# Kernel tuning notes

Hardware: AMD Instinct MI355X
Metric: run time of the kernel (lower is better)

Reference implementation:

```python
import jax, jax.numpy as jnp
import numpy as np

B, T, D, H = 8, 512, 1024, 16
DH = D // H
MAX_LEN = 512  # max_pos_encoding


def rel_pos_encoding(seq_len, dim):
    # Relative sinusoidal PE, full (non-causal) context, no hidden state.
    # positions: max_len-1 ... 1, 0, -1 ... -(max_len-1)
    pos = jnp.concatenate([
        jnp.arange(MAX_LEN - 1, 0, -1, dtype=jnp.float32),
        jnp.arange(0, -MAX_LEN, -1, dtype=jnp.float32),
    ])  # (2*max_len-1,)
    inv_freq = jnp.power(10000.0, -2.0 * jnp.arange(dim // 2, dtype=jnp.float32) / dim)
    ang = pos[:, None] * inv_freq[None, :]  # (2M-1, D/2)
    pe = jnp.zeros((2 * MAX_LEN - 1, dim), dtype=jnp.float32)
    pe = pe.at[:, 0::2].set(jnp.sin(ang)).at[:, 1::2].set(jnp.cos(ang))
    # non-causal slice: [max_len - seq_len : max_len - 1 + seq_len] -> 2T-1 rows
    return pe[MAX_LEN - seq_len: MAX_LEN - 1 + seq_len]


def rel_to_abs(s):
    # full-context skewing (Bello et al.): s is (B, H, T1, T2) with T2 = 2*T1 - 1
    b, h, t1, t2 = s.shape
    s = jnp.pad(s, ((0, 0), (0, 0), (0, 0), (0, 1)))
    s = s.reshape(b, h, t1 * (t2 + 1))
    s = jnp.pad(s, ((0, 0), (0, 0), (0, t2 - t1)))
    s = s.reshape(b, h, t1 + 1, t2)
    return s[:, :, :t1, t1 - 1:]  # (B, H, T1, T1)


def setup_inputs() -> dict:
    key = jax.random.key(0)
    ks = jax.random.split(key, 9)
    sc = 1.0 / np.sqrt(D)
    return {
        "x": jax.random.normal(ks[0], (B, T, D), dtype=jnp.float32),
        "Wq": jax.random.normal(ks[1], (D, D), dtype=jnp.float32) * sc,
        "bq": jnp.zeros((D,), dtype=jnp.float32),
        "Wk": jax.random.normal(ks[2], (D, D), dtype=jnp.float32) * sc,
        "bk": jnp.zeros((D,), dtype=jnp.float32),
        "Wv": jax.random.normal(ks[3], (D, D), dtype=jnp.float32) * sc,
        "bv": jnp.zeros((D,), dtype=jnp.float32),
        "Wp": jax.random.normal(ks[4], (D, D), dtype=jnp.float32) * sc,
        "bp": jnp.zeros((D,), dtype=jnp.float32),
        "Wo": jax.random.normal(ks[5], (D, D), dtype=jnp.float32) * sc,
        "bo": jnp.zeros((D,), dtype=jnp.float32),
        "u": jax.random.normal(ks[6], (D,), dtype=jnp.float32) * 0.02,
        "v": jax.random.normal(ks[7], (D,), dtype=jnp.float32) * 0.02,
    }


def reference(x, Wq, bq, Wk, bk, Wv, bv, Wp, bp, Wo, bo, u, v):
    b, t, d = x.shape
    Q = x @ Wq.T + bq
    K = x @ Wk.T + bk
    V = x @ Wv.T + bv
    Qu = Q + u
    Qv = Q + v
    # relative positional embeddings, projected: (2T-1, D)
    E = rel_pos_encoding(t, d) @ Wp.T + bp
    # split heads
    Qu = Qu.reshape(b, t, H, DH).transpose(0, 2, 1, 3)  # (B,H,T,dh)
    Qv = Qv.reshape(b, t, H, DH).transpose(0, 2, 1, 3)
    Kh = K.reshape(b, t, H, DH).transpose(0, 2, 1, 3)
    Vh = V.reshape(b, t, H, DH).transpose(0, 2, 1, 3)
    Eh = E.reshape(2 * t - 1, H, DH)  # (R,H,dh)
    att_scores_K = jnp.einsum("bhqd,bhkd->bhqk", Qu, Kh)
    att_scores_E = rel_to_abs(jnp.einsum("bhqd,rhd->bhqr", Qv, Eh))
    att_scores = (att_scores_K + att_scores_E) / jnp.sqrt(jnp.float32(DH))
    att_w = jax.nn.softmax(att_scores, axis=-1)
    O = jnp.einsum("bhqk,bhkd->bhqd", att_w, Vh)
    O = O.transpose(0, 2, 1, 3).reshape(b, t, d)
    return O @ Wo.T + bo
```

## Files before the change

### kernel.cpp

```cpp
#include <hip/hip_runtime.h>
#include <hip/hip_bf16.h>
#include <cmath>

using short8  = __attribute__((ext_vector_type(8))) short;
using f32x4   = __attribute__((ext_vector_type(4))) float;
using uint4v  = __attribute__((ext_vector_type(4))) unsigned;

#define DEV static __device__ __forceinline__

DEV unsigned short f2bf(float f) {
  union { float f; unsigned u; } v; v.f = f;
  unsigned r = v.u + 0x7FFFu + ((v.u >> 16) & 1u);
  return (unsigned short)(r >> 16);
}
DEV float bf2f(unsigned short b) {
  union { unsigned u; float f; } v; v.u = ((unsigned)b) << 16;
  return v.f;
}

DEV void async_copy16(const void* g, void* l) {
  __builtin_amdgcn_global_load_lds(
      (const __attribute__((address_space(1))) void*)g,
      (__attribute__((address_space(3))) void*)l, 16, 0, 0);
}

#define DPPF(x, ctrl)                                                     \
  __builtin_bit_cast(float, __builtin_amdgcn_update_dpp(                  \
      __builtin_bit_cast(int, (x)), __builtin_bit_cast(int, (x)), (ctrl), \
      0xF, 0xF, false))

DEV float rowmax16(float t) {
  t = fmaxf(t, DPPF(t, 0x128));
  t = fmaxf(t, DPPF(t, 0x124));
  t = fmaxf(t, DPPF(t, 0x122));
  t = fmaxf(t, DPPF(t, 0x121));
  return t;
}
DEV float rowsum16(float t) {
  t += DPPF(t, 0x128);
  t += DPPF(t, 0x124);
  t += DPPF(t, 0x122);
  t += DPPF(t, 0x121);
  return t;
}
DEV unsigned dpp_xor8(unsigned x) {
  return (unsigned)__builtin_amdgcn_update_dpp((int)x, (int)x, 0x128, 0xF, 0xF, false);
}

__global__ __launch_bounds__(256) void prep_kernel(
    const float* __restrict__ x,  const float* __restrict__ Wq,
    const float* __restrict__ Wk, const float* __restrict__ Wv,
    const float* __restrict__ Wp, const float* __restrict__ Wo,
    const float* __restrict__ bq, const float* __restrict__ bk,
    const float* __restrict__ bv,
    unsigned short* __restrict__ xb, unsigned short* __restrict__ Wqkvb,
    unsigned short* __restrict__ Wpb, unsigned short* __restrict__ Wob,
    unsigned short* __restrict__ peb, float* __restrict__ bqkv) {
  const int blk = blockIdx.x;
  const int tid = threadIdx.x;
  if (blk < 9216) {
    const float* src;
    unsigned short* dst;
    int i;
    if (blk < 4096) {
      src = x; dst = xb; i = blk * 256 + tid;
    } else {
      const int w = (blk - 4096) >> 10;
      i = ((blk - 4096) & 1023) * 256 + tid;
      if      (w == 0) { src = Wq; dst = Wqkvb; }
      else if (w == 1) { src = Wk; dst = Wqkvb + 1048576; }
      else if (w == 2) { src = Wv; dst = Wqkvb + 2097152; }
      else if (w == 3) { src = Wp; dst = Wpb; }
      else             { src = Wo; dst = Wob; }
    }
    float4 v = ((const float4*)src)[i];
    ushort4 o;
    o.x = f2bf(v.x); o.y = f2bf(v.y); o.z = f2bf(v.z); o.w = f2bf(v.w);
    ((ushort4*)dst)[i] = o;
  } else if (blk < 11264) {
    const int idx = (blk - 9216) * 256 + tid;
    const int r = idx >> 9;
    const int m = idx & 511;
    const float inv_freq = __expf((float)m * -0.017988946039016004f);
    const float ang = (float)(511 - r) * inv_freq;
    peb[(size_t)r * 1024 + 2 * m]     = f2bf(sinf(ang));
    peb[(size_t)r * 1024 + 2 * m + 1] = f2bf(cosf(ang));
  } else {
    const int i = (blk - 11264) * 256 + tid;
    const float* s = (i < 1024) ? bq : (i < 2048) ? bk : bv;
    bqkv[i] = s[i & 1023];
  }
}

template <int OUTF32>
DEV void gemm_tile(const unsigned short* __restrict__ A,
                   const unsigned short* __restrict__ B,
                   const float* __restrict__ bias, void* __restrict__ Cout,
                   int N, int K, int m0, int n0, int tid,
                   unsigned short* sA, unsigned short* sB) {
  const int lane = tid & 63;
  const int wave = tid >> 6;

  const unsigned short* gA[4];
  const unsigned short* gB[4];
  unsigned ldst[4];
#pragma unroll
  for (int it = 0; it < 4; ++it) {
    unsigned o = (unsigned)(it * 4096 + wave * 1024 + lane * 16);
    unsigned row = o >> 7;
    unsigned x = (o & 127u) ^ ((row & 7u) << 4);
    ldst[it] = it * 4096 + wave * 1024;
    gA[it] = A + (size_t)(m0 + (int)row) * K + (x >> 1);
    gB[it] = B + (size_t)(n0 + (int)row) * K + (x >> 1);
  }

  f32x4 acc[4][4];
#pragma unroll
  for (int i = 0; i < 4; ++i)
#pragma unroll
    for (int j = 0; j < 4; ++j) acc[i][j] = f32x4{0.f, 0.f, 0.f, 0.f};

  const int wm = (wave >> 1) << 6;
  const int wn = (wave & 1) << 6;
  const int rsel = lane & 15;
  const int g = lane >> 4;
  const int ksel = g << 4;

#pragma unroll
  for (int it = 0; it < 4; ++it) {
    async_copy16(gA[it], (char*)sA + ldst[it]);
    async_copy16(gB[it], (char*)sB + ldst[it]);
  }

  int cur = 0;
  for (int k0 = 0; k0 < K; k0 += 64) {
    __syncthreads();
    if (k0 + 64 < K) {
#pragma unroll
      for (int it = 0; it < 4; ++it) {
        async_copy16(gA[it] + k0 + 64, (char*)sA + (cur ^ 1) * 16384 + ldst[it]);
        async_copy16(gB[it] + k0 + 64, (char*)sB + (cur ^ 1) * 16384 + ldst[it]);
      }
    }
    const char* sAc = (const char*)sA + cur * 16384;
    const char* sBc = (const char*)sB + cur * 16384;
    __builtin_amdgcn_s_setprio(1);
#pragma unroll
    for (int kb = 0; kb < 2; ++kb) {
      const int kbyte = kb * 64 + ksel;
      short8 af[4], bf8[4];
#pragma unroll
      for (int i = 0; i < 4; ++i) {
        const int ra = wm + i * 16 + rsel;
        af[i] = *(const short8*)(sAc + ra * 128 + (kbyte ^ ((ra & 7) << 4)));
        const int rb = wn + i * 16 + rsel;
        bf8[i] = *(const short8*)(sBc + rb * 128 + (kbyte ^ ((rb & 7) << 4)));
      }
#pragma unroll
      for (int i = 0; i < 4; ++i)
#pragma unroll
        for (int j = 0; j < 4; ++j)
          acc[i][j] = __builtin_amdgcn_mfma_f32_16x16x32_bf16(bf8[j], af[i], acc[i][j], 0, 0, 0);
    }
    __builtin_amdgcn_s_setprio(0);
    cur ^= 1;
  }

#pragma unroll
  for (int i = 0; i < 4; ++i) {
    const int row = m0 + wm + i * 16 + rsel;
#pragma unroll
    for (int j = 0; j < 4; ++j) {
      const int col0 = n0 + wn + j * 16 + 4 * g;
      const float4 bb = *(const float4*)(bias + col0);
      if (OUTF32) {
        float4 o;
        o.x = acc[i][j][0] + bb.x;
        o.y = acc[i][j][1] + bb.y;
        o.z = acc[i][j][2] + bb.z;
        o.w = acc[i][j][3] + bb.w;
        *(float4*)&((float*)Cout)[(size_t)row * N + col0] = o;
      } else {
        ushort4 o;
        o.x = f2bf(acc[i][j][0] + bb.x);
        o.y = f2bf(acc[i][j][1] + bb.y);
        o.z = f2bf(acc[i][j][2] + bb.z);
        o.w = f2bf(acc[i][j][3] + bb.w);
        *(ushort4*)&((unsigned short*)Cout)[(size_t)row * N + col0] = o;
      }
    }
  }
}

__global__ __launch_bounds__(256) void gemm_qkv_e_kernel(
    const unsigned short* __restrict__ xb, const unsigned short* __restrict__ Wqkvb,
    const float* __restrict__ bqkv, unsigned short* __restrict__ QKVb,
    const unsigned short* __restrict__ peb, const unsigned short* __restrict__ Wpb,
    const float* __restrict__ bp, unsigned short* __restrict__ Eb) {
  __shared__ unsigned short sA[2 * 128 * 64];
  __shared__ unsigned short sB[2 * 128 * 64];
  const int cpx = 104;
  const int bid = (blockIdx.x & 7) * cpx + (blockIdx.x >> 3);
  if (bid < 768) {
    const int mt = bid / 24, nt = bid - mt * 24;
    gemm_tile<0>(xb, Wqkvb, bqkv, QKVb, 3072, 1024, mt << 7, nt << 7,
                 threadIdx.x, sA, sB);
  } else {
    const int b2 = bid - 768;
    gemm_tile<0>(peb, Wpb, bp, Eb, 1024, 1024, (b2 >> 3) << 7, (b2 & 7) << 7,
                 threadIdx.x, sA, sB);
  }
}

__global__ __launch_bounds__(256) void gemm_out_kernel(
    const unsigned short* __restrict__ Ob, const unsigned short* __restrict__ Wob,
    const float* __restrict__ bo, float* __restrict__ out) {
  __shared__ unsigned short sA[2 * 128 * 64];
  __shared__ unsigned short sB[2 * 128 * 64];
  const int cpx = 32;
  const int bid = (blockIdx.x & 7) * cpx + (blockIdx.x >> 3);
  gemm_tile<1>(Ob, Wob, bo, out, 1024, 1024, (bid >> 3) << 7, (bid & 7) << 7,
               threadIdx.x, sA, sB);
}

__global__ __launch_bounds__(256, 2) void attn_kernel(
    const unsigned short* __restrict__ QKV,
    const unsigned short* __restrict__ E,
    const float* __restrict__ uvec, const float* __restrict__ vvec,
    unsigned short* __restrict__ O) {
  __shared__ unsigned short sK[2 * 4096];
  __shared__ unsigned short sE[4 * 4096];
  __shared__ unsigned short sVt[2 * 4096];
  __shared__ unsigned short sP[4][2048];

  const int tid = threadIdx.x;
  const int lane = tid & 63;
  const int wave = tid >> 6;
  const int cpx = gridDim.x >> 3;
  const int bid = (blockIdx.x & 7) * cpx + (blockIdx.x >> 3);
  const int qt = bid & 3;
  const int h = (bid >> 2) & 15;
  const int b = bid >> 6;
  const int q0 = qt << 7;

  const int rsel = lane & 15;
  const int g = lane >> 4;
  const int ilocb = g << 2;
  const int cb0 = 96 - 32 * wave;

  const unsigned short* Qb = QKV + (size_t)b * 512 * 3072 + h * 64;
  const unsigned short* Kb = Qb + 1024;
  const unsigned short* Vb = Qb + 2048;

  const float sc = 0.125f * 1.44269504088896f;

  short8 v8b[2];
#pragma unroll
  for (int it = 0; it < 2; ++it) {
    const int c = it * 256 + tid;
    v8b[it] = *(const short8*)(Vb + (size_t)(c >> 3) * 3072 + ((c & 7) << 3));
  }
#pragma unroll
  for (int it = 0; it < 2; ++it) {
    const unsigned o = (unsigned)(it * 4096 + wave * 1024 + lane * 16);
    const unsigned row = o >> 7;
    const unsigned x = (o & 127u) ^ ((row & 7u) << 4);
    async_copy16(Kb + (size_t)row * 3072 + (x >> 1),
                 (char*)sK + it * 4096 + wave * 1024);
  }
#pragma unroll
  for (int hh = 0; hh < 3; ++hh) {
    const int H = 6 - 2 * qt + hh;
#pragma unroll
    for (int it = 0; it < 2; ++it) {
      const unsigned o = (unsigned)(it * 4096 + wave * 1024 + lane * 16);
      const unsigned row = o >> 7;
      const unsigned x = (o & 127u) ^ ((row & 7u) << 4);
      async_copy16(E + (size_t)(H * 64 + (int)row) * 1024 + h * 64 + (x >> 1),
                   (char*)sE + (H & 3) * 8192 + it * 4096 + wave * 1024);
    }
  }

  short8 aU[2][2], aV[2][2];
#pragma unroll
  for (int f = 0; f < 2; ++f) {
    const int qrow = q0 + 32 * wave + 16 * f + rsel;
    const int dob = g * 8;
#pragma unroll
    for (int kb = 0; kb < 2; ++kb) {
      short8 q8 = *(const short8*)(Qb + (size_t)qrow * 3072 + kb * 32 + dob);
#pragma unroll
      for (int j = 0; j < 8; ++j) {
        const float qf = bf2f((unsigned short)q8[j]);
        aU[f][kb][j] = (short)f2bf((qf + uvec[h * 64 + kb * 32 + dob + j]) * sc);
        aV[f][kb][j] = (short)f2bf((qf + vvec[h * 64 + kb * 32 + dob + j]) * sc);
      }
    }
  }

#pragma unroll
  for (int it = 0; it < 2; ++it) {
    const int c = it * 256 + tid;
    const int trow = c >> 3;
    const int db = (c & 7) << 3;
    const int odd = trow & 1;
    const int kp = (trow & ~1) * 2;
    const uint4v dw = __builtin_bit_cast(uint4v, v8b[it]);
#pragma unroll
    for (int p = 0; p < 4; ++p) {
      const unsigned mine = dw[p];
      const unsigned other = dpp_xor8(mine);
      const unsigned res = odd ? ((mine & 0xffff0000u) | (other >> 16))
                               : ((other << 16) | (mine & 0xffffu));
      const int d = db + 2 * p + odd;
      *(unsigned*)((char*)sVt + d * 128 + (kp ^ (((d ^ (d >> 3)) & 7) << 4))) = res;
    }
  }
#pragma unroll
  for (int it = 0; it < 2; ++it) {
    const int c = it * 256 + tid;
    v8b[it] = *(const short8*)(Vb + (size_t)(64 + (c >> 3)) * 3072 + ((c & 7) << 3));
  }

  int srcLn[4];
  bool hiSel[4];
#pragma unroll
  for (int r = 0; r < 4; ++r) {
    const int offs = 15 - (ilocb + r) + rsel;
    srcLn[r] = (lane & 48) | (offs & 15);
    hiSel[r] = offs >= 16;
  }

  float mrun[2][4], lrun[2][4];
  f32x4 oacc[2][4];
#pragma unroll
  for (int f = 0; f < 2; ++f)
#pragma unroll
    for (int r = 0; r < 4; ++r) { mrun[f][r] = -INFINITY; lrun[f][r] = 0.f; }
#pragma unroll
  for (int f = 0; f < 2; ++f)
#pragma unroll
    for (int n = 0; n < 4; ++n) oacc[f][n] = f32x4{0.f, 0.f, 0.f, 0.f};

  for (int kt = 0; kt < 8; ++kt) {
    const int k0 = kt << 6;
    const int cur = kt & 1;
    const int H0 = 6 - 2 * qt + kt;

    __syncthreads();

    if (kt < 7) {
      const int kn = k0 + 64;
#pragma unroll
      for (int it = 0; it < 2; ++it) {
        const unsigned o = (unsigned)(it * 4096 + wave * 1024 + lane * 16);
        const unsigned row = o >> 7;
        const unsigned x = (o & 127u) ^ ((row & 7u) << 4);
        async_copy16(Kb + (size_t)(kn + (int)row) * 3072 + (x >> 1),
                     (char*)sK + (cur ^ 1) * 8192 + it * 4096 + wave * 1024);
      }
      {
        const int H = H0 + 3;
#pragma unroll
        for (int it = 0; it < 2; ++it) {
          const unsigned o = (unsigned)(it * 4096 + wave * 1024 + lane * 16);
          const unsigned row = o >> 7;
          const unsigned x = (o & 127u) ^ ((row & 7u) << 4);
          async_copy16(E + (size_t)(H * 64 + (int)row) * 1024 + h * 64 + (x >> 1),
                       (char*)sE + (H & 3) * 8192 + it * 4096 + wave * 1024);
        }
      }
#pragma unroll
      for (int it = 0; it < 2; ++it) {
        const int c = it * 256 + tid;
        const int trow = c >> 3;
        const int db = (c & 7) << 3;
        const int odd = trow & 1;
        const int kp = (trow & ~1) * 2;
        const uint4v dw = __builtin_bit_cast(uint4v, v8b[it]);
#pragma unroll
        for (int p = 0; p < 4; ++p) {
          const unsigned mine = dw[p];
          const unsigned other = dpp_xor8(mine);
          const unsigned res = odd ? ((mine & 0xffff0000u) | (other >> 16))
                                   : ((other << 16) | (mine & 0xffffu));
          const int d = db + 2 * p + odd;
          *(unsigned*)((char*)sVt + (cur ^ 1) * 8192 + d * 128 +
                       (kp ^ (((d ^ (d >> 3)) & 7) << 4))) = res;
        }
      }
    }

    f32x4 skacc[2][4], gacc[2][5];
#pragma unroll
    for (int f = 0; f < 2; ++f) {
#pragma unroll
      for (int nf = 0; nf < 4; ++nf) skacc[f][nf] = f32x4{0.f, 0.f, 0.f, 0.f};
#pragma unroll
      for (int cf = 0; cf < 5; ++cf) gacc[f][cf] = f32x4{0.f, 0.f, 0.f, 0.f};
    }

    __builtin_amdgcn_s_setprio(1);
#pragma unroll
    for (int kb = 0; kb < 2; ++kb) {
      const int kbyte = kb * 64 + g * 16;
      const char* sKc = (const char*)sK + cur * 8192;
      short8 ka, kbb;
      {
        const int r0 = rsel, r1 = 16 + rsel;
        ka  = *(const short8*)(sKc + r0 * 128 + (kbyte ^ ((r0 & 7) << 4)));
        kbb = *(const short8*)(sKc + r1 * 128 + (kbyte ^ ((r1 & 7) << 4)));
      }
      skacc[0][0] = __builtin_amdgcn_mfma_f32_16x16x32_bf16(aU[0][kb], ka,  skacc[0][0], 0, 0, 0);
      skacc[1][0] = __builtin_amdgcn_mfma_f32_16x16x32_bf16(aU[1][kb], ka,  skacc[1][0], 0, 0, 0);
      skacc[0][1] = __builtin_amdgcn_mfma_f32_16x16x32_bf16(aU[0][kb], kbb, skacc[0][1], 0, 0, 0);
      skacc[1][1] = __builtin_amdgcn_mfma_f32_16x16x32_bf16(aU[1][kb], kbb, skacc[1][1], 0, 0, 0);
      {
        const int r0 = 32 + rsel, r1 = 48 + rsel;
        ka  = *(const short8*)(sKc + r0 * 128 + (kbyte ^ ((r0 & 7) << 4)));
        kbb = *(const short8*)(sKc + r1 * 128 + (kbyte ^ ((r1 & 7) << 4)));
      }
      skacc[0][2] = __builtin_amdgcn_mfma_f32_16x16x32_bf16(aU[0][kb], ka,  skacc[0][2], 0, 0, 0);
      skacc[1][2] = __builtin_amdgcn_mfma_f32_16x16x32_bf16(aU[1][kb], ka,  skacc[1][2], 0, 0, 0);
      skacc[0][3] = __builtin_amdgcn_mfma_f32_16x16x32_bf16(aU[0][kb], kbb, skacc[0][3], 0, 0, 0);
      skacc[1][3] = __builtin_amdgcn_mfma_f32_16x16x32_bf16(aU[1][kb], kbb, skacc[1][3], 0, 0, 0);
    }
    __builtin_amdgcn_sched_barrier(0);

    if (kt < 6) {
#pragma unroll
      for (int it = 0; it < 2; ++it) {
        const int c = it * 256 + tid;
        v8b[it] = *(const short8*)(Vb + (size_t)(k0 + 128 + (c >> 3)) * 3072 +
                                   ((c & 7) << 3));
      }
    }

#pragma unroll
    for (int kb = 0; kb < 2; ++kb) {
      const int kbyte = kb * 64 + g * 16;
      short8 e0, e1, e2;
#define LDE(cfu)                                                              \
  ({                                                                          \
    const int rowbase = cb0 + 16 * (cfu);                                     \
    const int rb = rowbase + rsel;                                            \
    const int slot = (H0 + (rowbase >> 6)) & 3;                               \
    *(const short8*)((const char*)sE + slot * 8192 + (rb & 63) * 128 +        \
                     (kbyte ^ ((rb & 7) << 4)));                              \
  })
      e0 = LDE(0); e1 = LDE(1); e2 = LDE(2);
      gacc[1][0] = __builtin_amdgcn_mfma_f32_16x16x32_bf16(aV[1][kb], e0, gacc[1][0], 0, 0, 0);
      gacc[0][0] = __builtin_amdgcn_mfma_f32_16x16x32_bf16(aV[0][kb], e1, gacc[0][0], 0, 0, 0);
      gacc[1][1] = __builtin_amdgcn_mfma_f32_16x16x32_bf16(aV[1][kb], e1, gacc[1][1], 0, 0, 0);
      gacc[0][1] = __builtin_amdgcn_mfma_f32_16x16x32_bf16(aV[0][kb], e2, gacc[0][1], 0, 0, 0);
      gacc[1][2] = __builtin_amdgcn_mfma_f32_16x16x32_bf16(aV[1][kb], e2, gacc[1][2], 0, 0, 0);
      e0 = LDE(3); e1 = LDE(4); e2 = LDE(5);
      gacc[0][2] = __builtin_amdgcn_mfma_f32_16x16x32_bf16(aV[0][kb], e0, gacc[0][2], 0, 0, 0);
      gacc[1][3] = __builtin_amdgcn_mfma_f32_16x16x32_bf16(aV[1][kb], e0, gacc[1][3], 0, 0, 0);
      gacc[0][3] = __builtin_amdgcn_mfma_f32_16x16x32_bf16(aV[0][kb], e1, gacc[0][3], 0, 0, 0);
      gacc[1][4] = __builtin_amdgcn_mfma_f32_16x16x32_bf16(aV[1][kb], e1, gacc[1][4], 0, 0, 0);
      gacc[0][4] = __builtin_amdgcn_mfma_f32_16x16x32_bf16(aV[0][kb], e2, gacc[0][4], 0, 0, 0);
#undef LDE
    }
    __builtin_amdgcn_s_setprio(0);

#pragma unroll
    for (int f = 0; f < 2; ++f)
#pragma unroll
      for (int r = 0; r < 4; ++r) {
        float gsh[5];
#pragma unroll
        for (int cf = 0; cf < 5; ++cf)
          gsh[cf] = __shfl(gacc[f][cf][r], srcLn[r], 64);
#pragma unroll
        for (int nf = 0; nf < 4; ++nf)
          skacc[f][nf][r] += hiSel[r] ? gsh[nf + 1] : gsh[nf];
      }

    float scl[2][4];
#pragma unroll
    for (int f = 0; f < 2; ++f) {
      float rsum[4];
#pragma unroll
      for (int r = 0; r < 4; ++r) {
        float t = fmaxf(fmaxf(skacc[f][0][r], skacc[f][1][r]),
                        fmaxf(skacc[f][2][r], skacc[f][3][r]));
        t = rowmax16(t);
        const float mnew = fmaxf(mrun[f][r], t);
        scl[f][r] = __builtin_amdgcn_exp2f(mrun[f][r] - mnew);
        mrun[f][r] = mnew;
        rsum[r] = 0.f;
      }
#pragma unroll
      for (int nf = 0; nf < 4; ++nf)
#pragma unroll
        for (int r = 0; r < 4; ++r) {
          const float p = __builtin_amdgcn_exp2f(skacc[f][nf][r] - mrun[f][r]);
          rsum[r] += p;
          const int rloc = 16 * f + ilocb + r;
          const int jb = (nf * 16 + rsel) * 2;
          *(unsigned short*)((char*)sP[wave] + rloc * 128 +
                             (jb ^ ((rloc & 7) << 4))) = f2bf(p);
        }
#pragma unroll
      for (int r = 0; r < 4; ++r)
        lrun[f][r] = lrun[f][r] * scl[f][r] + rowsum16(rsum[r]);
#pragma unroll
      for (int nf = 0; nf < 4; ++nf)
#pragma unroll
        for (int r = 0; r < 4; ++r) oacc[f][nf][r] *= scl[f][r];
    }

    __builtin_amdgcn_s_setprio(1);
#pragma unroll
    for (int kb = 0; kb < 2; ++kb) {
      const int kbyte = kb * 64 + g * 16;
      short8 ap[2];
#pragma unroll
      for (int f = 0; f < 2; ++f) {
        const int pr = 16 * f + rsel;
        ap[f] = *(const short8*)((const char*)sP[wave] + pr * 128 +
                                 (kbyte ^ ((pr & 7) << 4)));
      }
#pragma unroll
      for (int nf = 0; nf < 4; ++nf) {
        const int rv = nf * 16 + rsel;
        short8 vb8 = *(const short8*)((const char*)sVt + cur * 8192 + rv * 128 +
                                      (kbyte ^ (((rv ^ (rv >> 3)) & 7) << 4)));
#pragma unroll
        for (int f = 0; f < 2; ++f)
          oacc[f][nf] = __builtin_amdgcn_mfma_f32_16x16x32_bf16(
              ap[f], vb8, oacc[f][nf], 0, 0, 0);
      }
    }
    __builtin_amdgcn_s_setprio(0);
  }

#pragma unroll
  for (int f = 0; f < 2; ++f)
#pragma unroll
    for (int nf = 0; nf < 4; ++nf)
#pragma unroll
      for (int r = 0; r < 4; ++r) {
        const int t = q0 + 32 * wave + 16 * f + ilocb + r;
        const int col = h * 64 + nf * 16 + rsel;
        O[(size_t)(b * 512 + t) * 1024 + col] = f2bf(oacc[f][nf][r] / lrun[f][r]);
      }
}

extern "C" void kernel_launch(void* const* d_in, const int* in_sizes, int n_in,
                              void* d_out, int out_size, void* d_ws, size_t ws_size,
                              hipStream_t stream) {
  const float* x  = (const float*)d_in[0];
  const float* Wq = (const float*)d_in[1];
  const float* bq = (const float*)d_in[2];
  const float* Wk = (const float*)d_in[3];
  const float* bk = (const float*)d_in[4];
  const float* Wv = (const float*)d_in[5];
  const float* bv = (const float*)d_in[6];
  const float* Wp = (const float*)d_in[7];
  const float* bp = (const float*)d_in[8];
  const float* Wo = (const float*)d_in[9];
  const float* bo = (const float*)d_in[10];
  const float* u  = (const float*)d_in[11];
  const float* v  = (const float*)d_in[12];
  float* out = (float*)d_out;

  char* ws = (char*)d_ws;
  const size_t MB = 1024 * 1024;
  unsigned short* xb    = (unsigned short*)(ws);
  unsigned short* Wqkvb = (unsigned short*)(ws + 8 * MB);
  unsigned short* Wpb   = (unsigned short*)(ws + 14 * MB);
  unsigned short* Wob   = (unsigned short*)(ws + 16 * MB);
  unsigned short* peb   = (unsigned short*)(ws + 18 * MB);
  unsigned short* QKVb  = (unsigned short*)(ws + 20 * MB);
  unsigned short* Eb    = (unsigned short*)(ws + 44 * MB);
  unsigned short* Ob    = (unsigned short*)(ws + 46 * MB);
  float* bqkv           = (float*)(ws + 54 * MB);

  prep_kernel<<<dim3(11276), dim3(256), 0, stream>>>(
      x, Wq, Wk, Wv, Wp, Wo, bq, bk, bv, xb, Wqkvb, Wpb, Wob, peb, bqkv);

  gemm_qkv_e_kernel<<<dim3(832), dim3(256), 0, stream>>>(
      xb, Wqkvb, bqkv, QKVb, peb, Wpb, bp, Eb);
  attn_kernel<<<dim3(512), dim3(256), 0, stream>>>(QKVb, Eb, u, v, Ob);
  gemm_out_kernel<<<dim3(256), dim3(256), 0, stream>>>(Ob, Wob, bo, out);
}
```

Baseline: 112.2 us.

## Use 256x128 tiles with 512-thread blocks for QKV/E projection GEMM

Replaces the 128x128, 256-thread, double-buffered tile in the fused QKV and positional projection GEMM with a 256x128 tile run by 8 waves. It uses single-buffered LDS with barriers before and after each K-step. The launch halves to 416 blocks of 512 threads. The goal is more operand reuse per block and more resident waves per CU to hide latency. In exchange it gives up the explicit prefetch overlap of the next K-slice. The output GEMM keeps the old tile, now as a separate f32-output function.

```diff
diff --git a/kernel.cpp b/kernel.cpp
--- a/kernel.cpp
+++ b/kernel.cpp
@@ -92,12 +92,120 @@
   }
 }
 
-template <int OUTF32>
-DEV void gemm_tile(const unsigned short* __restrict__ A,
-                   const unsigned short* __restrict__ B,
-                   const float* __restrict__ bias, void* __restrict__ Cout,
-                   int N, int K, int m0, int n0, int tid,
-                   unsigned short* sA, unsigned short* sB) {
+DEV void gemm_tile256(const unsigned short* __restrict__ A,
+                      const unsigned short* __restrict__ B,
+                      const float* __restrict__ bias,
+                      unsigned short* __restrict__ Cout,
+                      int N, int K, int m0, int n0, int tid,
+                      unsigned short* sA, unsigned short* sB) {
+  const int lane = tid & 63;
+  const int wave = tid >> 6;
+
+  const unsigned short* gA[4];
+  unsigned ldstA[4];
+#pragma unroll
+  for (int it = 0; it < 4; ++it) {
+    unsigned o = (unsigned)(it * 8192 + wave * 1024 + lane * 16);
+    unsigned row = o >> 7;
+    unsigned x = (o & 127u) ^ ((row & 7u) << 4);
+    ldstA[it] = o;
+    gA[it] = A + (size_t)(m0 + (int)row) * K + (x >> 1);
+  }
+  const unsigned short* gB[2];
+  unsigned ldstB[2];
+#pragma unroll
+  for (int it = 0; it < 2; ++it) {
+    unsigned o = (unsigned)(it * 8192 + wave * 1024 + lane * 16);
+    unsigned row = o >> 7;
+    unsigned x = (o & 127u) ^ ((row & 7u) << 4);
+    ldstB[it] = o;
+    gB[it] = B + (size_t)(n0 + (int)row) * K + (x >> 1);
+  }
+
+  f32x4 acc[4][4];
+#pragma unroll
+  for (int i = 0; i < 4; ++i)
+#pragma unroll
+    for (int j = 0; j < 4; ++j) acc[i][j] = f32x4{0.f, 0.f, 0.f, 0.f};
+
+  const int wm = (wave >> 1) << 6;
+  const int wn = (wave & 1) << 6;
+  const int rsel = lane & 15;
+  const int g = lane >> 4;
+  const int ksel = g << 4;
+
+  for (int k0 = 0; k0 < K; k0 += 64) {
+#pragma unroll
+    for (int it = 0; it < 4; ++it)
+      async_copy16(gA[it] + k0, (char*)sA + ldstA[it]);
+#pragma unroll
+    for (int it = 0; it < 2; ++it)
+      async_copy16(gB[it] + k0, (char*)sB + ldstB[it]);
+    __syncthreads();
+    __builtin_amdgcn_s_setprio(1);
+#pragma unroll
+    for (int kb = 0; kb < 2; ++kb) {
+      const int kbyte = kb * 64 + ksel;
+      short8 af[4], bf8[4];
+#pragma unroll
+      for (int i = 0; i < 4; ++i) {
+        const int ra = wm + i * 16 + rsel;
+        af[i] = *(const short8*)((const char*)sA + ra * 128 + (kbyte ^ ((ra & 7) << 4)));
+        const int rb = wn + i * 16 + rsel;
+        bf8[i] = *(const short8*)((const char*)sB + rb * 128 + (kbyte ^ ((rb & 7) << 4)));
+      }
+#pragma unroll
+      for (int i = 0; i < 4; ++i)
+#pragma unroll
+        for (int j = 0; j < 4; ++j)
+          acc[i][j] = __builtin_amdgcn_mfma_f32_16x16x32_bf16(bf8[j], af[i], acc[i][j], 0, 0, 0);
+    }
+    __builtin_amdgcn_s_setprio(0);
+    __syncthreads();
+  }
+
+#pragma unroll
+  for (int i = 0; i < 4; ++i) {
+    const int row = m0 + wm + i * 16 + rsel;
+#pragma unroll
+    for (int j = 0; j < 4; ++j) {
+      const int col0 = n0 + wn + j * 16 + 4 * g;
+      const float4 bb = *(const float4*)(bias + col0);
+      ushort4 o;
+      o.x = f2bf(acc[i][j][0] + bb.x);
+      o.y = f2bf(acc[i][j][1] + bb.y);
+      o.z = f2bf(acc[i][j][2] + bb.z);
+      o.w = f2bf(acc[i][j][3] + bb.w);
+      *(ushort4*)&Cout[(size_t)row * N + col0] = o;
+    }
+  }
+}
+
+__global__ __launch_bounds__(512, 2) void gemm_qkv_e_kernel(
+    const unsigned short* __restrict__ xb, const unsigned short* __restrict__ Wqkvb,
+    const float* __restrict__ bqkv, unsigned short* __restrict__ QKVb,
+    const unsigned short* __restrict__ peb, const unsigned short* __restrict__ Wpb,
+    const float* __restrict__ bp, unsigned short* __restrict__ Eb) {
+  __shared__ unsigned short sA[256 * 64];
+  __shared__ unsigned short sB[128 * 64];
+  const int cpx = 52;
+  const int bid = (blockIdx.x & 7) * cpx + (blockIdx.x >> 3);
+  if (bid < 384) {
+    const int mt = bid / 24, nt = bid - mt * 24;
+    gemm_tile256(xb, Wqkvb, bqkv, QKVb, 3072, 1024, mt << 8, nt << 7,
+                 threadIdx.x, sA, sB);
+  } else {
+    const int b2 = bid - 384;
+    gemm_tile256(peb, Wpb, bp, Eb, 1024, 1024, (b2 >> 3) << 8, (b2 & 7) << 7,
+                 threadIdx.x, sA, sB);
+  }
+}
+
+DEV void gemm_tile_f32(const unsigned short* __restrict__ A,
+                       const unsigned short* __restrict__ B,
+                       const float* __restrict__ bias, float* __restrict__ Cout,
+                       int N, int K, int m0, int n0, int tid,
+                       unsigned short* sA, unsigned short* sB) {
   const int lane = tid & 63;
   const int wave = tid >> 6;
 
@@ -131,7 +239,6 @@
     async_copy16(gA[it], (char*)sA + ldst[it]);
     async_copy16(gB[it], (char*)sB + ldst[it]);
   }
-
   int cur = 0;
   for (int k0 = 0; k0 < K; k0 += 64) {
     __syncthreads();
@@ -173,42 +280,13 @@
     for (int j = 0; j < 4; ++j) {
       const int col0 = n0 + wn + j * 16 + 4 * g;
       const float4 bb = *(const float4*)(bias + col0);
-      if (OUTF32) {
-        float4 o;
-        o.x = acc[i][j][0] + bb.x;
-        o.y = acc[i][j][1] + bb.y;
-        o.z = acc[i][j][2] + bb.z;
-        o.w = acc[i][j][3] + bb.w;
-        *(float4*)&((float*)Cout)[(size_t)row * N + col0] = o;
-      } else {
-        ushort4 o;
-        o.x = f2bf(acc[i][j][0] + bb.x);
-        o.y = f2bf(acc[i][j][1] + bb.y);
-        o.z = f2bf(acc[i][j][2] + bb.z);
-        o.w = f2bf(acc[i][j][3] + bb.w);
-        *(ushort4*)&((unsigned short*)Cout)[(size_t)row * N + col0] = o;
-      }
-    }
-  }
-}
-
-__global__ __launch_bounds__(256) void gemm_qkv_e_kernel(
-    const unsigned short* __restrict__ xb, const unsigned short* __restrict__ Wqkvb,
-    const float* __restrict__ bqkv, unsigned short* __restrict__ QKVb,
-    const unsigned short* __restrict__ peb, const unsigned short* __restrict__ Wpb,
-    const float* __restrict__ bp, unsigned short* __restrict__ Eb) {
-  __shared__ unsigned short sA[2 * 128 * 64];
-  __shared__ unsigned short sB[2 * 128 * 64];
-  const int cpx = 104;
-  const int bid = (blockIdx.x & 7) * cpx + (blockIdx.x >> 3);
-  if (bid < 768) {
-    const int mt = bid / 24, nt = bid - mt * 24;
-    gemm_tile<0>(xb, Wqkvb, bqkv, QKVb, 3072, 1024, mt << 7, nt << 7,
-                 threadIdx.x, sA, sB);
-  } else {
-    const int b2 = bid - 768;
-    gemm_tile<0>(peb, Wpb, bp, Eb, 1024, 1024, (b2 >> 3) << 7, (b2 & 7) << 7,
-                 threadIdx.x, sA, sB);
+      float4 o;
+      o.x = acc[i][j][0] + bb.x;
+      o.y = acc[i][j][1] + bb.y;
+      o.z = acc[i][j][2] + bb.z;
+      o.w = acc[i][j][3] + bb.w;
+      *(float4*)&Cout[(size_t)row * N + col0] = o;
+    }
   }
 }
 
@@ -219,8 +297,8 @@
   __shared__ unsigned short sB[2 * 128 * 64];
   const int cpx = 32;
   const int bid = (blockIdx.x & 7) * cpx + (blockIdx.x >> 3);
-  gemm_tile<1>(Ob, Wob, bo, out, 1024, 1024, (bid >> 3) << 7, (bid & 7) << 7,
-               threadIdx.x, sA, sB);
+  gemm_tile_f32(Ob, Wob, bo, out, 1024, 1024, (bid >> 3) << 7, (bid & 7) << 7,
+                threadIdx.x, sA, sB);
 }
 
 __global__ __launch_bounds__(256, 2) void attn_kernel(
@@ -581,7 +659,7 @@
   prep_kernel<<<dim3(11276), dim3(256), 0, stream>>>(
       x, Wq, Wk, Wv, Wp, Wo, bq, bk, bv, xb, Wqkvb, Wpb, Wob, peb, bqkv);
 
-  gemm_qkv_e_kernel<<<dim3(832), dim3(256), 0, stream>>>(
+  gemm_qkv_e_kernel<<<dim3(416), dim3(512), 0, stream>>>(
       xb, Wqkvb, bqkv, QKVb, peb, Wpb, bp, Eb);
   attn_kernel<<<dim3(512), dim3(256), 0, stream>>>(QKVb, Eb, u, v, Ob);
   gemm_out_kernel<<<dim3(256), dim3(256), 0, stream>>>(Ob, Wob, bo, out);
```

Result: slower. 126.7 us (+12.9%).
